# Kernel optimization log

Hardware: AMD Instinct MI355X
Metric: run time of the kernel (lower is better)

## Reference

```python
import jax, jax.numpy as jnp
import numpy as np
from jax import lax

EPS = 1e-5
BETA = 0.2  # commitment loss weight


def _conv(x, w, b, stride=2, pad=1):
    # torch Conv2d(k=4, s=2, p=1), NCHW / OIHW
    y = lax.conv_general_dilated(x, w, (stride, stride), [(pad, pad), (pad, pad)],
                                 dimension_numbers=('NCHW', 'OIHW', 'NCHW'))
    return y + b[None, :, None, None]


def _convT(x, w, b):
    # torch ConvTranspose2d(k=4, s=2, p=1): dilated conv with flipped kernel,
    # effective pad = k - 1 - p = 2. w is torch layout [in, out, kH, kW].
    wt = jnp.flip(w, (2, 3)).transpose(1, 0, 2, 3)  # -> [out, in, kH, kW]
    y = lax.conv_general_dilated(x, wt, (1, 1), [(2, 2), (2, 2)], lhs_dilation=(2, 2),
                                 dimension_numbers=('NCHW', 'OIHW', 'NCHW'))
    return y + b[None, :, None, None]


def _bn(x, g, b):
    # BatchNorm2d in training mode: per-channel batch statistics (biased var)
    m = x.mean((0, 2, 3), keepdims=True)
    v = x.var((0, 2, 3), keepdims=True)
    xn = (x - m) * lax.rsqrt(v + EPS)
    return g[None, :, None, None] * xn + b[None, :, None, None]


def _forward(x, enc_w1, enc_b1, enc_w2, enc_b2, enc_w3, enc_b3,
             enc_g1, enc_be1, enc_g2, enc_be2, enc_g3, enc_be3,
             codebook,
             dec_w1, dec_b1, dec_w2, dec_b2, dec_w3, dec_b3,
             dec_g1, dec_be1, dec_g2, dec_be2, dec_g3, dec_be3):
    # ---- Encoder: [B,1,256,256] -> [B,32,32,32] ----
    h = jax.nn.relu(_bn(_conv(x, enc_w1, enc_b1), enc_g1, enc_be1))
    h = jax.nn.relu(_bn(_conv(h, enc_w2, enc_b2), enc_g2, enc_be2))
    q_in = jax.nn.relu(_bn(_conv(h, enc_w3, enc_b3), enc_g3, enc_be3))

    B, C, H, W = q_in.shape
    # ---- Quantiser: cdist + argmin + codebook gather ----
    z = q_in.transpose(0, 2, 3, 1).reshape(B, H * W, C)  # [B, HW, C]
    # squared euclidean distance (same argmin as torch.cdist)
    d2 = (jnp.sum(z * z, -1, keepdims=True)
          - 2.0 * jnp.einsum('bnc,kc->bnk', z, codebook)
          + jnp.sum(codebook * codebook, -1))  # [B, HW, K]
    idx = jnp.argmin(d2, axis=-1)  # [B, HW] int
    q_out = codebook[idx].reshape(B, H, W, C).transpose(0, 3, 1, 2)  # [B,C,H,W]

    commitment = jnp.mean((lax.stop_gradient(q_out) - q_in) ** 2)
    codebook_l = jnp.mean((q_out - lax.stop_gradient(q_in)) ** 2)
    quant_loss = codebook_l + BETA * commitment
    # straight-through estimator
    q_st = q_in + lax.stop_gradient(q_out - q_in)
    encoding_indices = idx.reshape(-1, H, W)

    # ---- Decoder: [B,32,32,32] -> [B,1,256,256] ----
    d = jax.nn.relu(_bn(_convT(q_st, dec_w1, dec_b1), dec_g1, dec_be1))
    d = jax.nn.relu(_bn(_convT(d, dec_w2, dec_b2), dec_g2, dec_be2))
    out = _bn(_convT(d, dec_w3, dec_b3), dec_g3, dec_be3)

    recon = jnp.mean((x - out) ** 2)
    total_loss = quant_loss + recon
    return out, total_loss, encoding_indices


def setup_inputs() -> dict:
    key = jax.random.key(0)
    ks = jax.random.split(key, 12)
    rn = lambda k, s, sc=0.05: jax.random.normal(k, s, jnp.float32) * sc
    inp = {
        'x': jax.random.normal(ks[0], (64, 1, 256, 256), jnp.float32),
        'enc_w1': rn(ks[1], (16, 1, 4, 4)),  'enc_b1': jnp.zeros((16,), jnp.float32),
        'enc_w2': rn(ks[2], (16, 16, 4, 4)), 'enc_b2': jnp.zeros((16,), jnp.float32),
        'enc_w3': rn(ks[3], (32, 16, 4, 4)), 'enc_b3': jnp.zeros((32,), jnp.float32),
        'enc_g1': jnp.ones((16,), jnp.float32), 'enc_be1': jnp.zeros((16,), jnp.float32),
        'enc_g2': jnp.ones((16,), jnp.float32), 'enc_be2': jnp.zeros((16,), jnp.float32),
        'enc_g3': jnp.ones((32,), jnp.float32), 'enc_be3': jnp.zeros((32,), jnp.float32),
        'codebook': jax.random.normal(ks[4], (512, 32), jnp.float32),  # nn.Embedding ~ N(0,1)
        'dec_w1': rn(ks[5], (32, 16, 4, 4)), 'dec_b1': jnp.zeros((16,), jnp.float32),  # [in,out,kH,kW]
        'dec_w2': rn(ks[6], (16, 16, 4, 4)), 'dec_b2': jnp.zeros((16,), jnp.float32),
        'dec_w3': rn(ks[7], (16, 1, 4, 4)),  'dec_b3': jnp.zeros((1,), jnp.float32),
        'dec_g1': jnp.ones((16,), jnp.float32), 'dec_be1': jnp.zeros((16,), jnp.float32),
        'dec_g2': jnp.ones((16,), jnp.float32), 'dec_be2': jnp.zeros((16,), jnp.float32),
        'dec_g3': jnp.ones((1,), jnp.float32),  'dec_be3': jnp.zeros((1,), jnp.float32),
    }
    return inp


def reference(x, enc_w1, enc_b1, enc_w2, enc_b2, enc_w3, enc_b3,
              enc_g1, enc_be1, enc_g2, enc_be2, enc_g3, enc_be3,
              codebook,
              dec_w1, dec_b1, dec_w2, dec_b2, dec_w3, dec_b3,
              dec_g1, dec_be1, dec_g2, dec_be2, dec_g3, dec_be3):
    return _forward(x, enc_w1, enc_b1, enc_w2, enc_b2, enc_w3, enc_b3,
                    enc_g1, enc_be1, enc_g2, enc_be2, enc_g3, enc_be3,
                    codebook,
                    dec_w1, dec_b1, dec_w2, dec_b2, dec_w3, dec_b3,
                    dec_g1, dec_be1, dec_g2, dec_be2, dec_g3, dec_be3)
```

## Files before the change

kernel.cpp:

```cpp
#include <hip/hip_runtime.h>

#define BLK 256


template<int CO>
__device__ __forceinline__ void block_stats(const float* acc, float* partOut) {
  __shared__ float red[2][CO][4];
  const int lane = threadIdx.x & 63;
  const int wv   = threadIdx.x >> 6;
#pragma unroll
  for (int co = 0; co < CO; ++co) {
    float s = acc[co];
    float q = s * s;
#pragma unroll
    for (int off = 32; off > 0; off >>= 1) {
      s += __shfl_down(s, off, 64);
      q += __shfl_down(q, off, 64);
    }
    if (lane == 0) { red[0][co][wv] = s; red[1][co][wv] = q; }
  }
  __syncthreads();
  if (threadIdx.x < CO) {
    const int co = threadIdx.x;
    float s = red[0][co][0] + red[0][co][1] + red[0][co][2] + red[0][co][3];
    float q = red[1][co][0] + red[1][co][1] + red[1][co][2] + red[1][co][3];
    partOut[co * 2]     = s;
    partOut[co * 2 + 1] = q;
  }
}

__device__ __forceinline__ void block_stats2(float s, float q, float* partOut) {
  __shared__ float red2[2][4];
  const int lane = threadIdx.x & 63;
  const int wv   = threadIdx.x >> 6;
#pragma unroll
  for (int off = 32; off > 0; off >>= 1) {
    s += __shfl_down(s, off, 64);
    q += __shfl_down(q, off, 64);
  }
  if (lane == 0) { red2[0][wv] = s; red2[1][wv] = q; }
  __syncthreads();
  if (threadIdx.x == 0) {
    partOut[0] = red2[0][0] + red2[0][1] + red2[0][2] + red2[0][3];
    partOut[1] = red2[1][0] + red2[1][1] + red2[1][2] + red2[1][3];
  }
}


__global__ __launch_bounds__(BLK) void twc_k(const float* __restrict__ w,
                                             float* __restrict__ wt,
                                             int CI, int CO) {
  const int total = CI * CO * 16;
  for (int i = threadIdx.x; i < total; i += BLK) {
    const int co = i % CO;
    const int rest = i / CO;
    const int kw = rest & 3, kh = (rest >> 2) & 3, ci = rest >> 4;
    wt[i] = w[(co * CI + ci) * 16 + kh * 4 + kw];
  }
}

__global__ __launch_bounds__(BLK) void twt_k(const float* __restrict__ w,
                                             float* __restrict__ wt,
                                             int CI, int CO) {
  const int total = CI * CO * 16;
  for (int i = threadIdx.x; i < total; i += BLK) {
    const int co = i % CO;
    const int rest = i / CO;
    const int kw = rest & 3, kh = (rest >> 2) & 3, ci = rest >> 4;
    wt[i] = w[(ci * CO + co) * 16 + kh * 4 + kw];
  }
}


template<int CI, int CO, int HIN, int WIN, bool BN_IN>
__global__ __launch_bounds__(BLK) void conv_s(
    const float* __restrict__ in, const float* __restrict__ wt,
    const float* __restrict__ bias,
    const float* __restrict__ scIn, const float* __restrict__ shIn,
    float* __restrict__ out, float* __restrict__ part)
{
  constexpr int HOUT = HIN / 2, WOUT = WIN / 2;
  float sc[CI], sh[CI];
  if constexpr (BN_IN) {
#pragma unroll
    for (int ci = 0; ci < CI; ++ci) { sc[ci] = scIn[ci]; sh[ci] = shIn[ci]; }
  }

  const int idx = blockIdx.x * BLK + threadIdx.x;
  const int ow  = idx % WOUT;
  const int oh  = (idx / WOUT) % HOUT;
  const int b   = idx / (WOUT * HOUT);

  float acc[CO];
#pragma unroll
  for (int co = 0; co < CO; ++co) acc[co] = bias[co];

  const float* inb = in + (size_t)b * CI * HIN * WIN;

#pragma unroll
  for (int kh = 0; kh < 4; ++kh) {
    const int ih = oh * 2 - 1 + kh;
    if ((unsigned)ih < (unsigned)HIN) {
#pragma unroll
      for (int kw = 0; kw < 4; ++kw) {
        const int iw = ow * 2 - 1 + kw;
        if ((unsigned)iw < (unsigned)WIN) {
#pragma unroll 2
          for (int ci = 0; ci < CI; ++ci) {
            float v = inb[(ci * HIN + ih) * WIN + iw];
            if constexpr (BN_IN) v = fmaxf(fmaf(sc[ci], v, sh[ci]), 0.f);
            const float* wrow = wt + ((ci * 4 + kh) * 4 + kw) * CO;
#pragma unroll
            for (int co = 0; co < CO; ++co)
              acc[co] = fmaf(v, wrow[co], acc[co]);
          }
        }
      }
    }
  }

#pragma unroll
  for (int co = 0; co < CO; ++co)
    out[((size_t)(b * CO + co) * HOUT + oh) * WOUT + ow] = acc[co];

  block_stats<CO>(acc, part + (size_t)blockIdx.x * CO * 2);
}


template<int CI, int CO, int HIN, int WIN, bool BN_IN>
__global__ __launch_bounds__(BLK) void convT_s(
    const float* __restrict__ in, const float* __restrict__ wt,
    const float* __restrict__ bias,
    const float* __restrict__ scIn, const float* __restrict__ shIn,
    float* __restrict__ out, float* __restrict__ part)
{
  constexpr int HOUT = HIN * 2, WOUT = WIN * 2;
  float sc[CI], sh[CI];
  if constexpr (BN_IN) {
#pragma unroll
    for (int ci = 0; ci < CI; ++ci) { sc[ci] = scIn[ci]; sh[ci] = shIn[ci]; }
  }

  const int idx = blockIdx.x * BLK + threadIdx.x;
  const int ow  = idx % WOUT;
  const int oh  = (idx / WOUT) % HOUT;
  const int b   = idx / (WOUT * HOUT);

  float acc[CO];
#pragma unroll
  for (int co = 0; co < CO; ++co) acc[co] = bias[co];

  const float* inb = in + (size_t)b * CI * HIN * WIN;
  const int kh0 = 1 - (oh & 1);
  const int kw0 = 1 - (ow & 1);

#pragma unroll
  for (int th = 0; th < 2; ++th) {
    const int kh  = kh0 + 2 * th;
    const int ihh = oh + 1 - kh;
    const int ih  = ihh >> 1;
    if (ihh >= 0 && ih < HIN) {
#pragma unroll
      for (int tw = 0; tw < 2; ++tw) {
        const int kw  = kw0 + 2 * tw;
        const int iww = ow + 1 - kw;
        const int iw  = iww >> 1;
        if (iww >= 0 && iw < WIN) {
#pragma unroll 2
          for (int ci = 0; ci < CI; ++ci) {
            float v = inb[(ci * HIN + ih) * WIN + iw];
            if constexpr (BN_IN) v = fmaxf(fmaf(sc[ci], v, sh[ci]), 0.f);
            const float* wrow = wt + ((ci * 4 + kh) * 4 + kw) * CO;
#pragma unroll
            for (int co = 0; co < CO; ++co)
              acc[co] = fmaf(v, wrow[co], acc[co]);
          }
        }
      }
    }
  }

#pragma unroll
  for (int co = 0; co < CO; ++co)
    out[((size_t)(b * CO + co) * HOUT + oh) * WOUT + ow] = acc[co];

  block_stats<CO>(acc, part + (size_t)blockIdx.x * CO * 2);
}


__global__ __launch_bounds__(BLK) void convT3q_k(
    const float* __restrict__ in, const float* __restrict__ w,
    const float* __restrict__ bias,
    const float* __restrict__ scIn, const float* __restrict__ shIn,
    float* __restrict__ out, float* __restrict__ part)
{
  __shared__ float wl[256];
  wl[threadIdx.x] = w[threadIdx.x];
  float sc[16], sh[16];
#pragma unroll
  for (int ci = 0; ci < 16; ++ci) { sc[ci] = scIn[ci]; sh[ci] = shIn[ci]; }
  const float b0 = bias[0];
  __syncthreads();

  const int idx = blockIdx.x * BLK + threadIdx.x;
  const int tx = idx & 63;
  const int ty = (idx >> 6) & 63;
  const int b  = idx >> 12;
  const int i0 = ty * 2, j0 = tx * 2;

  constexpr int TAP[4][4] = {{1,1,3,0},{0,2,2,1},{1,2,3,1},{0,3,2,2}};

  float acc[4][4];
#pragma unroll
  for (int r = 0; r < 4; ++r)
#pragma unroll
    for (int c = 0; c < 4; ++c) acc[r][c] = b0;

  const float* inb = in + (size_t)b * 16 * 16384;

#pragma unroll 4
  for (int ci = 0; ci < 16; ++ci) {
    const float sci = sc[ci], shi = sh[ci];
    const float* base = inb + ci * 16384;
    float v[4][4];
#pragma unroll
    for (int pr = 0; pr < 4; ++pr) {
      const int ih = i0 - 1 + pr;
      const bool okr = (unsigned)ih < 128u;
#pragma unroll
      for (int pc = 0; pc < 4; ++pc) {
        const int iw = j0 - 1 + pc;
        float val = 0.f;
        if (okr && (unsigned)iw < 128u)
          val = fmaxf(fmaf(sci, base[ih * 128 + iw], shi), 0.f);
        v[pr][pc] = val;
      }
    }
    const float4 w0 = *(const float4*)&wl[ci * 16 + 0];
    const float4 w1 = *(const float4*)&wl[ci * 16 + 4];
    const float4 w2 = *(const float4*)&wl[ci * 16 + 8];
    const float4 w3 = *(const float4*)&wl[ci * 16 + 12];
    const float wg[16] = {w0.x,w0.y,w0.z,w0.w, w1.x,w1.y,w1.z,w1.w,
                          w2.x,w2.y,w2.z,w2.w, w3.x,w3.y,w3.z,w3.w};
#pragma unroll
    for (int r = 0; r < 4; ++r) {
      const int k1r = TAP[r][0], p1r = TAP[r][1], k2r = TAP[r][2], p2r = TAP[r][3];
#pragma unroll
      for (int c = 0; c < 4; ++c) {
        const int k1c = TAP[c][0], p1c = TAP[c][1], k2c = TAP[c][2], p2c = TAP[c][3];
        float a = acc[r][c];
        a = fmaf(v[p1r][p1c], wg[k1r * 4 + k1c], a);
        a = fmaf(v[p1r][p2c], wg[k1r * 4 + k2c], a);
        a = fmaf(v[p2r][p1c], wg[k2r * 4 + k1c], a);
        a = fmaf(v[p2r][p2c], wg[k2r * 4 + k2c], a);
        acc[r][c] = a;
      }
    }
  }

  float* ob = out + (size_t)b * 65536;
#pragma unroll
  for (int r = 0; r < 4; ++r) {
    float4 o;
    o.x = acc[r][0]; o.y = acc[r][1]; o.z = acc[r][2]; o.w = acc[r][3];
    *(float4*)&ob[(ty * 4 + r) * 256 + tx * 4] = o;
  }

  float s = 0.f, q = 0.f;
#pragma unroll
  for (int r = 0; r < 4; ++r)
#pragma unroll
    for (int c = 0; c < 4; ++c) { s += acc[r][c]; q = fmaf(acc[r][c], acc[r][c], q); }
  block_stats2(s, q, part + (size_t)blockIdx.x * 2);
}


template<int C>
__global__ __launch_bounds__(BLK) void stats_k(
    const float* __restrict__ part, int nB, double N,
    const float* __restrict__ g, const float* __restrict__ be,
    float* __restrict__ sc, float* __restrict__ sh)
{
  const int c = blockIdx.x;
  double s0 = 0.0, s1 = 0.0;
  for (int i = threadIdx.x; i < nB; i += BLK) {
    s0 += (double)part[(size_t)i * C * 2 + c * 2];
    s1 += (double)part[(size_t)i * C * 2 + c * 2 + 1];
  }
  __shared__ double lds[8];
  const int lane = threadIdx.x & 63, wv = threadIdx.x >> 6;
#pragma unroll
  for (int off = 32; off > 0; off >>= 1) {
    s0 += __shfl_down(s0, off, 64);
    s1 += __shfl_down(s1, off, 64);
  }
  if (lane == 0) { lds[wv * 2] = s0; lds[wv * 2 + 1] = s1; }
  __syncthreads();
  if (threadIdx.x == 0) {
    s0 = lds[0] + lds[2] + lds[4] + lds[6];
    s1 = lds[1] + lds[3] + lds[5] + lds[7];
    const double mean = s0 / N;
    const double var  = s1 / N - mean * mean;
    const double inv  = 1.0 / sqrt(var + 1e-5);
    sc[c] = (float)((double)g[c] * inv);
    sh[c] = (float)((double)be[c] - mean * (double)g[c] * inv);
  }
}


__global__ __launch_bounds__(BLK) void cbn_k(const float* __restrict__ cbg,
                                             float* __restrict__ cbn)
{
  const int k = blockIdx.x * BLK + threadIdx.x;
  float s = 0.f;
#pragma unroll
  for (int c = 0; c < 32; ++c) {
    const float x = cbg[k * 32 + c];
    s = fmaf(x, x, s);
  }
  cbn[k] = s;
}

__global__ __launch_bounds__(BLK) void quantp_k(
    const float* __restrict__ y3, const float* __restrict__ cbg,
    const float* __restrict__ cbnG,
    const float* __restrict__ sc, const float* __restrict__ sh,
    float* __restrict__ bd, int* __restrict__ bki)
{
  __shared__ float cb[64 * 32];
  __shared__ float cbnl[64];
  const int pblk  = blockIdx.x & 63;
  const int chunk = blockIdx.x >> 6;
  for (int i = threadIdx.x; i < 2048; i += BLK) cb[i] = cbg[chunk * 2048 + i];
  if (threadIdx.x < 64) cbnl[threadIdx.x] = cbnG[chunk * 64 + threadIdx.x];
  __syncthreads();

  const int pos0 = pblk * 1024 + threadIdx.x;

  float z[4][32];
#pragma unroll
  for (int c = 0; c < 32; ++c) {
    const float s_ = sc[c], h_ = sh[c];
#pragma unroll
    for (int j = 0; j < 4; ++j) {
      const int pos = pos0 + j * 256;
      const int bb = pos >> 10, pp = pos & 1023;
      z[j][c] = fmaxf(fmaf(s_, y3[((size_t)(bb * 32 + c)) * 1024 + pp], h_), 0.f);
    }
  }

  float best[4] = {3.402823466e38f, 3.402823466e38f, 3.402823466e38f, 3.402823466e38f};
  int   bk[4]   = {0, 0, 0, 0};

  for (int k = 0; k < 64; ++k) {
    const float4* row = (const float4*)&cb[k * 32];
    float d[4] = {0.f, 0.f, 0.f, 0.f};
#pragma unroll
    for (int c4 = 0; c4 < 8; ++c4) {
      const float4 cc = row[c4];
#pragma unroll
      for (int j = 0; j < 4; ++j) {
        d[j] = fmaf(z[j][c4 * 4 + 0], cc.x, d[j]);
        d[j] = fmaf(z[j][c4 * 4 + 1], cc.y, d[j]);
        d[j] = fmaf(z[j][c4 * 4 + 2], cc.z, d[j]);
        d[j] = fmaf(z[j][c4 * 4 + 3], cc.w, d[j]);
      }
    }
    const float cl = cbnl[k];
    const int kk = chunk * 64 + k;
#pragma unroll
    for (int j = 0; j < 4; ++j) {
      const float dd = cl - 2.f * d[j];
      if (dd < best[j]) { best[j] = dd; bk[j] = kk; }
    }
  }

#pragma unroll
  for (int j = 0; j < 4; ++j) {
    const int pos = pos0 + j * 256;
    bd[chunk * 65536 + pos]  = best[j];
    bki[chunk * 65536 + pos] = bk[j];
  }
}

__global__ __launch_bounds__(BLK) void quantm_k(
    const float* __restrict__ y3, const float* __restrict__ cbg,
    const float* __restrict__ sc, const float* __restrict__ sh,
    const float* __restrict__ bd, const int* __restrict__ bki,
    float* __restrict__ qout, float* __restrict__ idx_out,
    float* __restrict__ pq)
{
  const int pos = blockIdx.x * BLK + threadIdx.x;
  float best = 3.402823466e38f;
  int bk = 0;
#pragma unroll
  for (int s = 0; s < 8; ++s) {
    const float d = bd[s * 65536 + pos];
    const int   k = bki[s * 65536 + pos];
    if (d < best) { best = d; bk = k; }
  }

  const int b = pos >> 10, p = pos & 1023;
  const float4* qrow = (const float4*)(cbg + (size_t)bk * 32);
  float msd = 0.f;
#pragma unroll
  for (int c4 = 0; c4 < 8; ++c4) {
    const float4 q4 = qrow[c4];
    const float qv[4] = {q4.x, q4.y, q4.z, q4.w};
#pragma unroll
    for (int u = 0; u < 4; ++u) {
      const int c = c4 * 4 + u;
      const float v  = y3[((size_t)(b * 32 + c)) * 1024 + p];
      const float zz = fmaxf(fmaf(sc[c], v, sh[c]), 0.f);
      const float qq = qv[u];
      qout[((size_t)(b * 32 + c)) * 1024 + p] = zz + (qq - zz);
      const float df = qq - zz;
      msd = fmaf(df, df, msd);
    }
  }
  idx_out[pos] = (float)bk;
  block_stats2(msd, 0.f, pq + (size_t)blockIdx.x * 2);
}


__global__ __launch_bounds__(BLK) void final4_k(
    const float* __restrict__ y6, const float* __restrict__ x,
    const float* __restrict__ sc, const float* __restrict__ sh,
    float* __restrict__ out, float* __restrict__ pr)
{
  const size_t i = ((size_t)blockIdx.x * BLK + threadIdx.x) * 4;
  const float s0 = sc[0], h0 = sh[0];
  const float4 yv = *(const float4*)(y6 + i);
  const float4 xv = *(const float4*)(x + i);
  float4 ov;
  ov.x = fmaf(s0, yv.x, h0);
  ov.y = fmaf(s0, yv.y, h0);
  ov.z = fmaf(s0, yv.z, h0);
  ov.w = fmaf(s0, yv.w, h0);
  *(float4*)(out + i) = ov;
  const float d0 = xv.x - ov.x, d1 = xv.y - ov.y, d2 = xv.z - ov.z, d3 = xv.w - ov.w;
  float s = d0 * d0;
  s = fmaf(d1, d1, s);
  s = fmaf(d2, d2, s);
  s = fmaf(d3, d3, s);
  block_stats2(s, 0.f, pr + (size_t)blockIdx.x * 2);
}


__global__ __launch_bounds__(BLK) void loss_k(
    const float* __restrict__ pq, const float* __restrict__ pr,
    float* __restrict__ lossOut)
{
  double s = 0.0, r = 0.0;
  for (int i = threadIdx.x; i < 256; i += BLK)  s += (double)pq[i * 2];
  for (int i = threadIdx.x; i < 4096; i += BLK) r += (double)pr[i * 2];
  __shared__ double lds[8];
  const int lane = threadIdx.x & 63, wv = threadIdx.x >> 6;
#pragma unroll
  for (int off = 32; off > 0; off >>= 1) {
    s += __shfl_down(s, off, 64);
    r += __shfl_down(r, off, 64);
  }
  if (lane == 0) { lds[wv * 2] = s; lds[wv * 2 + 1] = r; }
  __syncthreads();
  if (threadIdx.x == 0) {
    s = lds[0] + lds[2] + lds[4] + lds[6];
    r = lds[1] + lds[3] + lds[5] + lds[7];
    lossOut[0] = (float)(1.2 * (s / 2097152.0) + r / 4194304.0);
  }
}


extern "C" void kernel_launch(void* const* d_in, const int* in_sizes, int n_in,
                              void* d_out, int out_size, void* d_ws, size_t ws_size,
                              hipStream_t stream) {
  const float* x    = (const float*)d_in[0];
  const float* ew1  = (const float*)d_in[1];
  const float* eb1  = (const float*)d_in[2];
  const float* ew2  = (const float*)d_in[3];
  const float* eb2  = (const float*)d_in[4];
  const float* ew3  = (const float*)d_in[5];
  const float* eb3  = (const float*)d_in[6];
  const float* eg1  = (const float*)d_in[7];
  const float* ebe1 = (const float*)d_in[8];
  const float* eg2  = (const float*)d_in[9];
  const float* ebe2 = (const float*)d_in[10];
  const float* eg3  = (const float*)d_in[11];
  const float* ebe3 = (const float*)d_in[12];
  const float* cbk  = (const float*)d_in[13];
  const float* dw1  = (const float*)d_in[14];
  const float* db1  = (const float*)d_in[15];
  const float* dw2  = (const float*)d_in[16];
  const float* db2  = (const float*)d_in[17];
  const float* dw3  = (const float*)d_in[18];
  const float* db3  = (const float*)d_in[19];
  const float* dg1  = (const float*)d_in[20];
  const float* dbe1 = (const float*)d_in[21];
  const float* dg2  = (const float*)d_in[22];
  const float* dbe2 = (const float*)d_in[23];
  const float* dg3  = (const float*)d_in[24];
  const float* dbe3 = (const float*)d_in[25];

  float* ws = (float*)d_ws;
  float* outp = (float*)d_out;

  float* SC = ws;
  float* SH = ws + 192;
  float* P1 = ws + 1024;
  float* P2 = ws + 132096;
  float* P3 = ws + 164864;
  float* P4 = ws + 181248;
  float* P5 = ws + 214016;
  float* P6 = ws + 345088;
  float* Pq = ws + 377856;
  float* Pr = ws + 378368;
  float* CBN = ws + 411648;
  float* WT1  = ws + 412160;
  float* WT2  = WT1 + 256;
  float* WT3  = WT2 + 4096;
  float* WTD1 = WT3 + 8192;
  float* WTD2 = WTD1 + 8192;

  float* y1 = ws + 524288;
  float* y2 = y1 + 16777216;
  float* y3 = y2 + 4194304;
  float* qo = y3 + 2097152;
  float* y6 = qo + 2097152;
  float* y4 = y2;
  float* y5 = y1;
  float* bd  = y2;
  int*   bki = (int*)(y2 + 524288);

  float* sc1 = SC + 0,  *sh1 = SH + 0;
  float* sc2 = SC + 32, *sh2 = SH + 32;
  float* sc3 = SC + 64, *sh3 = SH + 64;
  float* sc4 = SC + 96, *sh4 = SH + 96;
  float* sc5 = SC + 128,*sh5 = SH + 128;
  float* sc6 = SC + 160,*sh6 = SH + 160;

  twc_k<<<1, BLK, 0, stream>>>(ew1, WT1, 1, 16);
  twc_k<<<1, BLK, 0, stream>>>(ew2, WT2, 16, 16);
  twc_k<<<1, BLK, 0, stream>>>(ew3, WT3, 16, 32);
  twt_k<<<1, BLK, 0, stream>>>(dw1, WTD1, 32, 16);
  twt_k<<<1, BLK, 0, stream>>>(dw2, WTD2, 16, 16);
  cbn_k<<<2, BLK, 0, stream>>>(cbk, CBN);

  conv_s<1, 16, 256, 256, false><<<4096, BLK, 0, stream>>>(x,  WT1, eb1, nullptr, nullptr, y1, P1);
  stats_k<16><<<16, BLK, 0, stream>>>(P1, 4096, 1048576.0, eg1, ebe1, sc1, sh1);
  conv_s<16, 16, 128, 128, true><<<1024, BLK, 0, stream>>>(y1, WT2, eb2, sc1, sh1, y2, P2);
  stats_k<16><<<16, BLK, 0, stream>>>(P2, 1024, 262144.0, eg2, ebe2, sc2, sh2);
  conv_s<16, 32, 64, 64, true><<<256, BLK, 0, stream>>>(y2, WT3, eb3, sc2, sh2, y3, P3);
  stats_k<32><<<32, BLK, 0, stream>>>(P3, 256, 65536.0, eg3, ebe3, sc3, sh3);

  quantp_k<<<512, BLK, 0, stream>>>(y3, cbk, CBN, sc3, sh3, bd, bki);
  quantm_k<<<256, BLK, 0, stream>>>(y3, cbk, sc3, sh3, bd, bki, qo, outp + 4194305, Pq);

  convT_s<32, 16, 32, 32, false><<<1024, BLK, 0, stream>>>(qo, WTD1, db1, nullptr, nullptr, y4, P4);
  stats_k<16><<<16, BLK, 0, stream>>>(P4, 1024, 262144.0, dg1, dbe1, sc4, sh4);
  convT_s<16, 16, 64, 64, true><<<4096, BLK, 0, stream>>>(y4, WTD2, db2, sc4, sh4, y5, P5);
  stats_k<16><<<16, BLK, 0, stream>>>(P5, 4096, 1048576.0, dg2, dbe2, sc5, sh5);
  convT3q_k<<<1024, BLK, 0, stream>>>(y5, dw3, db3, sc5, sh5, y6, P6);
  stats_k<1><<<1, BLK, 0, stream>>>(P6, 1024, 4194304.0, dg3, dbe3, sc6, sh6);

  final4_k<<<4096, BLK, 0, stream>>>(y6, x, sc6, sh6, outp, Pr);
  loss_k<<<1, BLK, 0, stream>>>(Pq, Pr, outp + 4194304);
}
```

Before: 674.8 us.

## Compute 2x2 output quad per thread in transposed convs with 3x3 input reuse

The two decoder transposed convolutions now have each thread compute all four output parity positions of a 2x2 quad. Each thread loads a shared 3x3 input neighbourhood once per input channel and applies the BN+ReLU once per loaded value, instead of every output pixel reloading its own four taps. Results are stored as float2 pairs, and per-channel partial sums are combined before the block reduction, with a quarter as many blocks launched. The cost is much higher register pressure (64 accumulators plus a 3x3 window) and fewer threads in flight, which could lower occupancy.

After: 672.6 us. Within noise of the previous version (-0.3%).

```diff
diff --git a/kernel.cpp b/kernel.cpp
--- a/kernel.cpp
+++ b/kernel.cpp
@@ -12,6 +12,33 @@
   for (int co = 0; co < CO; ++co) {
     float s = acc[co];
     float q = s * s;
+#pragma unroll
+    for (int off = 32; off > 0; off >>= 1) {
+      s += __shfl_down(s, off, 64);
+      q += __shfl_down(q, off, 64);
+    }
+    if (lane == 0) { red[0][co][wv] = s; red[1][co][wv] = q; }
+  }
+  __syncthreads();
+  if (threadIdx.x < CO) {
+    const int co = threadIdx.x;
+    float s = red[0][co][0] + red[0][co][1] + red[0][co][2] + red[0][co][3];
+    float q = red[1][co][0] + red[1][co][1] + red[1][co][2] + red[1][co][3];
+    partOut[co * 2]     = s;
+    partOut[co * 2 + 1] = q;
+  }
+}
+
+template<int CO>
+__device__ __forceinline__ void block_statsV(const float* s_, const float* q_,
+                                             float* partOut) {
+  __shared__ float red[2][CO][4];
+  const int lane = threadIdx.x & 63;
+  const int wv   = threadIdx.x >> 6;
+#pragma unroll
+  for (int co = 0; co < CO; ++co) {
+    float s = s_[co];
+    float q = q_[co];
 #pragma unroll
     for (int off = 32; off > 0; off >>= 1) {
       s += __shfl_down(s, off, 64);
@@ -127,64 +154,92 @@
 }
 
 
-template<int CI, int CO, int HIN, int WIN, bool BN_IN>
-__global__ __launch_bounds__(BLK) void convT_s(
+template<int CI, int HIN, bool BN_IN>
+__global__ __launch_bounds__(BLK) void convTq_k(
     const float* __restrict__ in, const float* __restrict__ wt,
     const float* __restrict__ bias,
     const float* __restrict__ scIn, const float* __restrict__ shIn,
     float* __restrict__ out, float* __restrict__ part)
 {
-  constexpr int HOUT = HIN * 2, WOUT = WIN * 2;
-  float sc[CI], sh[CI];
-  if constexpr (BN_IN) {
-#pragma unroll
-    for (int ci = 0; ci < CI; ++ci) { sc[ci] = scIn[ci]; sh[ci] = shIn[ci]; }
-  }
-
+  constexpr int WIN = HIN, HOUT = 2 * HIN, WOUT = 2 * WIN;
   const int idx = blockIdx.x * BLK + threadIdx.x;
-  const int ow  = idx % WOUT;
-  const int oh  = (idx / WOUT) % HOUT;
-  const int b   = idx / (WOUT * HOUT);
-
-  float acc[CO];
-#pragma unroll
-  for (int co = 0; co < CO; ++co) acc[co] = bias[co];
+  const int qw = idx % WIN;
+  const int qh = (idx / WIN) % HIN;
+  const int b  = idx / (WIN * HIN);
+
+  constexpr int KH[2][2] = {{1, 3}, {0, 2}};
+  constexpr int PR[2][2] = {{1, 0}, {2, 1}};
+
+  float acc[2][2][16];
+#pragma unroll
+  for (int co = 0; co < 16; ++co) {
+    const float bv = bias[co];
+    acc[0][0][co] = bv; acc[0][1][co] = bv;
+    acc[1][0][co] = bv; acc[1][1][co] = bv;
+  }
 
   const float* inb = in + (size_t)b * CI * HIN * WIN;
-  const int kh0 = 1 - (oh & 1);
-  const int kw0 = 1 - (ow & 1);
-
-#pragma unroll
-  for (int th = 0; th < 2; ++th) {
-    const int kh  = kh0 + 2 * th;
-    const int ihh = oh + 1 - kh;
-    const int ih  = ihh >> 1;
-    if (ihh >= 0 && ih < HIN) {
-#pragma unroll
-      for (int tw = 0; tw < 2; ++tw) {
-        const int kw  = kw0 + 2 * tw;
-        const int iww = ow + 1 - kw;
-        const int iw  = iww >> 1;
-        if (iww >= 0 && iw < WIN) {
+
 #pragma unroll 2
-          for (int ci = 0; ci < CI; ++ci) {
-            float v = inb[(ci * HIN + ih) * WIN + iw];
-            if constexpr (BN_IN) v = fmaxf(fmaf(sc[ci], v, sh[ci]), 0.f);
-            const float* wrow = wt + ((ci * 4 + kh) * 4 + kw) * CO;
-#pragma unroll
-            for (int co = 0; co < CO; ++co)
-              acc[co] = fmaf(v, wrow[co], acc[co]);
+  for (int ci = 0; ci < CI; ++ci) {
+    float sci, shi;
+    if constexpr (BN_IN) { sci = scIn[ci]; shi = shIn[ci]; }
+    const float* base = inb + ci * HIN * WIN;
+    float v[3][3];
+#pragma unroll
+    for (int pr = 0; pr < 3; ++pr) {
+      const int ih = qh - 1 + pr;
+      const bool okr = (unsigned)ih < (unsigned)HIN;
+#pragma unroll
+      for (int pc = 0; pc < 3; ++pc) {
+        const int iw = qw - 1 + pc;
+        float val = 0.f;
+        if (okr && (unsigned)iw < (unsigned)WIN) {
+          val = base[ih * WIN + iw];
+          if constexpr (BN_IN) val = fmaxf(fmaf(sci, val, shi), 0.f);
+        }
+        v[pr][pc] = val;
+      }
+    }
+#pragma unroll
+    for (int py = 0; py < 2; ++py)
+#pragma unroll
+      for (int tr = 0; tr < 2; ++tr) {
+        const int kh = KH[py][tr], pr_ = PR[py][tr];
+#pragma unroll
+        for (int px = 0; px < 2; ++px)
+#pragma unroll
+          for (int tc = 0; tc < 2; ++tc) {
+            const int kw = KH[px][tc], pc_ = PR[px][tc];
+            const float* wrow = wt + ((ci * 4 + kh) * 4 + kw) * 16;
+            const float pv = v[pr_][pc_];
+#pragma unroll
+            for (int co = 0; co < 16; ++co)
+              acc[py][px][co] = fmaf(pv, wrow[co], acc[py][px][co]);
           }
-        }
       }
-    }
-  }
-
-#pragma unroll
-  for (int co = 0; co < CO; ++co)
-    out[((size_t)(b * CO + co) * HOUT + oh) * WOUT + ow] = acc[co];
-
-  block_stats<CO>(acc, part + (size_t)blockIdx.x * CO * 2);
+  }
+
+  float* ob = out + (size_t)b * 16 * HOUT * WOUT;
+#pragma unroll
+  for (int co = 0; co < 16; ++co)
+#pragma unroll
+    for (int py = 0; py < 2; ++py) {
+      float2 o; o.x = acc[py][0][co]; o.y = acc[py][1][co];
+      *(float2*)&ob[((size_t)co * HOUT + 2 * qh + py) * WOUT + 2 * qw] = o;
+    }
+
+  float s[16], q[16];
+#pragma unroll
+  for (int co = 0; co < 16; ++co) {
+    float a = acc[0][0][co] + acc[0][1][co] + acc[1][0][co] + acc[1][1][co];
+    float qq = acc[0][0][co] * acc[0][0][co];
+    qq = fmaf(acc[0][1][co], acc[0][1][co], qq);
+    qq = fmaf(acc[1][0][co], acc[1][0][co], qq);
+    qq = fmaf(acc[1][1][co], acc[1][1][co], qq);
+    s[co] = a; q[co] = qq;
+  }
+  block_statsV<16>(s, q, part + (size_t)blockIdx.x * 32);
 }
 
 
@@ -555,10 +610,10 @@
   quantp_k<<<512, BLK, 0, stream>>>(y3, cbk, CBN, sc3, sh3, bd, bki);
   quantm_k<<<256, BLK, 0, stream>>>(y3, cbk, sc3, sh3, bd, bki, qo, outp + 4194305, Pq);
 
-  convT_s<32, 16, 32, 32, false><<<1024, BLK, 0, stream>>>(qo, WTD1, db1, nullptr, nullptr, y4, P4);
-  stats_k<16><<<16, BLK, 0, stream>>>(P4, 1024, 262144.0, dg1, dbe1, sc4, sh4);
-  convT_s<16, 16, 64, 64, true><<<4096, BLK, 0, stream>>>(y4, WTD2, db2, sc4, sh4, y5, P5);
-  stats_k<16><<<16, BLK, 0, stream>>>(P5, 4096, 1048576.0, dg2, dbe2, sc5, sh5);
+  convTq_k<32, 32, false><<<256, BLK, 0, stream>>>(qo, WTD1, db1, nullptr, nullptr, y4, P4);
+  stats_k<16><<<16, BLK, 0, stream>>>(P4, 256, 262144.0, dg1, dbe1, sc4, sh4);
+  convTq_k<16, 64, true><<<1024, BLK, 0, stream>>>(y4, WTD2, db2, sc4, sh4, y5, P5);
+  stats_k<16><<<16, BLK, 0, stream>>>(P5, 1024, 1048576.0, dg2, dbe2, sc5, sh5);
   convT3q_k<<<1024, BLK, 0, stream>>>(y5, dw3, db3, sc5, sh5, y6, P6);
   stats_k<1><<<1, BLK, 0, stream>>>(P6, 1024, 4194304.0, dg3, dbe3, sc6, sh6);
 
```
